# Kernel tuning notes

Hardware: AMD Instinct MI355X
Metric: run time of the kernel (lower is better)

The kernel has to match this reference:

```python
import jax, jax.numpy as jnp
import numpy as np

B, NW, WL, CH, D, H, L, FF = 8, 1024, 8, 4, 512, 8, 4, 2048
K = 512  # num_masked = int(0.5 * NW)
SCALE = (D // H) ** -0.5


def _ln(x, g, b):
    m = jnp.mean(x, -1, keepdims=True)
    v = jnp.var(x, -1, keepdims=True)
    return (x - m) * jax.lax.rsqrt(v + 1e-5) * g + b


def setup_inputs():
    key = jax.random.key(0)
    ks = jax.random.split(key, 16)
    n = lambda i, shape, s=0.02: jax.random.normal(ks[i], shape, jnp.float32) * s
    return {
        "seq": jax.random.normal(ks[0], (B, NW * WL, CH), jnp.float32),
        "mask_idx": jax.lax.top_k(jax.random.uniform(ks[1], (B, NW)), K)[1].astype(jnp.int32),
        "pos_embedding": n(2, (1, NW + 1, D)),
        "mask_token": jax.random.normal(ks[3], (D,), jnp.float32),
        "pln1_g": jnp.ones((WL * CH,)), "pln1_b": jnp.zeros((WL * CH,)),
        "W_emb": n(4, (WL * CH, D)), "b_emb": jnp.zeros((D,)),
        "pln2_g": jnp.ones((D,)), "pln2_b": jnp.zeros((D,)),
        "aln_g": jnp.ones((L, D)), "aln_b": jnp.zeros((L, D)),
        "Wqkv": n(5, (L, D, 3 * D)),
        "Wo": n(6, (L, D, D)),
        "fln_g": jnp.ones((L, D)), "fln_b": jnp.zeros((L, D)),
        "Wff1": n(7, (L, D, FF)), "bff1": jnp.zeros((L, FF)),
        "Wff2": n(8, (L, FF, D)), "bff2": jnp.zeros((L, D)),
        "oln_g": jnp.ones((D,)), "oln_b": jnp.zeros((D,)),
        "W_words": n(9, (D, WL * CH)), "b_words": jnp.zeros((WL * CH,)),
    }


def reference(seq, mask_idx, pos_embedding, mask_token, pln1_g, pln1_b, W_emb, b_emb,
              pln2_g, pln2_b, aln_g, aln_b, Wqkv, Wo, fln_g, fln_b, Wff1, bff1,
              Wff2, bff2, oln_g, oln_b, W_words, b_words):
    b = seq.shape[0]
    words = seq.reshape(b, NW, WL * CH)                       # to_patch: 'b (n w) c -> b n (w c)'
    pos = pos_embedding[:, 1:NW + 1]                          # [1, NW, D]
    tokens = _ln(_ln(words, pln1_g, pln1_b) @ W_emb + b_emb, pln2_g, pln2_b) + pos
    mask_tokens = mask_token + pos                            # [1, NW, D] broadcast over batch
    bool_mask = jnp.zeros((b, NW), bool).at[jnp.arange(b)[:, None], mask_idx].set(True)
    tokens = jnp.where(bool_mask[..., None], mask_tokens, tokens)

    def block(x, p):
        h = _ln(x, p["ag"], p["ab"])
        q, k, v = [t.reshape(b, NW, H, D // H) for t in jnp.split(h @ p["Wqkv"], 3, axis=-1)]
        attn = jax.nn.softmax(jnp.einsum("bihd,bjhd->bhij", q, k) * SCALE, axis=-1)
        o = jnp.einsum("bhij,bjhd->bihd", attn, v).reshape(b, NW, D)
        x = x + o @ p["Wo"]
        h = _ln(x, p["fg"], p["fb"])
        x = x + jax.nn.gelu(h @ p["W1"] + p["b1"]) @ p["W2"] + p["b2"]
        return x, None

    layer_params = {"ag": aln_g, "ab": aln_b, "Wqkv": Wqkv, "Wo": Wo,
                    "fg": fln_g, "fb": fln_b, "W1": Wff1, "b1": bff1,
                    "W2": Wff2, "b2": bff2}
    encoded, _ = jax.lax.scan(block, tokens, layer_params)
    encoded = _ln(encoded, oln_g, oln_b)

    idx = mask_idx[..., None]
    enc_m = jnp.take_along_axis(encoded, idx, axis=1)         # [b, K, D] gather of masked positions
    pred = jax.nn.softmax((enc_m @ W_words + b_words).reshape(b, K, WL, CH), axis=-1)
    labels = jnp.take_along_axis(words, idx, axis=1).reshape(b, K, WL, CH)
    return pred, labels
```

## Files before the change

### kernel.cpp

```cpp
#include <hip/hip_runtime.h>
#include <hip/hip_bf16.h>
#include <stdint.h>


#define NTOK 8192
#define DMODEL 512
#define NHEAD 8
#define DHEAD 64
#define NWIN 1024
#define NBATCH 8
#define KMASK 512
#define FFDIM 2048
#define NLAYER 4

typedef __bf16 bf16x8 __attribute__((ext_vector_type(8)));
typedef float f32x4 __attribute__((ext_vector_type(4)));

#define MFMA16(a, b, c) __builtin_amdgcn_mfma_f32_16x16x32_bf16(a, b, c, 0, 0, 0)

static __device__ __forceinline__ void gload_lds16(const void* g, void* l) {
    __builtin_amdgcn_global_load_lds(
        (const __attribute__((address_space(1))) uint32_t*)g,
        (__attribute__((address_space(3))) uint32_t*)l, 16, 0, 0);
}

static __device__ __forceinline__ float gelu_tanh(float v) {
    float x3 = v * v * v;
    return 0.5f * v * (1.f + tanhf(0.7978845608028654f * (v + 0.044715f * x3)));
}

__global__ void embed_kernel(const float* __restrict__ seq,
                             const float* __restrict__ pos_emb,
                             const float* __restrict__ pln1_g,
                             const float* __restrict__ pln1_b,
                             const float* __restrict__ W_emb,
                             const float* __restrict__ b_emb,
                             const float* __restrict__ pln2_g,
                             const float* __restrict__ pln2_b,
                             float* __restrict__ x) {
    int tok = blockIdx.x;
    int w = tok & (NWIN - 1);
    int t = threadIdx.x;

    __shared__ float wraw[32];
    __shared__ float ln1[32];
    __shared__ float red[256], red2[256];

    if (t < 32) wraw[t] = seq[(size_t)tok * 32 + t];
    __syncthreads();

    float m = 0.f;
    for (int j = 0; j < 32; j++) m += wraw[j];
    m *= (1.f / 32.f);
    float v = 0.f;
    for (int j = 0; j < 32; j++) { float d = wraw[j] - m; v += d * d; }
    v *= (1.f / 32.f);
    float rs = rsqrtf(v + 1e-5f);
    if (t < 32) ln1[t] = (wraw[t] - m) * rs * pln1_g[t] + pln1_b[t];
    __syncthreads();

    int c0 = t, c1 = t + 256;
    float e0 = b_emb[c0];
    float e1 = b_emb[c1];
    for (int j = 0; j < 32; j++) {
        float a = ln1[j];
        e0 += a * W_emb[j * DMODEL + c0];
        e1 += a * W_emb[j * DMODEL + c1];
    }

    red[t] = e0 + e1;
    red2[t] = e0 * e0 + e1 * e1;
    __syncthreads();
    for (int o = 128; o > 0; o >>= 1) {
        if (t < o) { red[t] += red[t + o]; red2[t] += red2[t + o]; }
        __syncthreads();
    }
    float mean = red[0] * (1.f / 512.f);
    float var = red2[0] * (1.f / 512.f) - mean * mean;
    float rs2 = rsqrtf(var + 1e-5f);

    const float* pr = pos_emb + (size_t)(1 + w) * DMODEL;
    x[(size_t)tok * DMODEL + c0] =
        (e0 - mean) * rs2 * pln2_g[c0] + pln2_b[c0] + pr[c0];
    x[(size_t)tok * DMODEL + c1] =
        (e1 - mean) * rs2 * pln2_g[c1] + pln2_b[c1] + pr[c1];
}

__global__ void mask_scatter_kernel(const int* __restrict__ mask_idx,
                                    const float* __restrict__ mask_token,
                                    const float* __restrict__ pos_emb,
                                    float* __restrict__ x) {
    int bk = blockIdx.x;
    int b = bk >> 9;
    int k = bk & 511;
    int idx = mask_idx[b * KMASK + k];
    int t = threadIdx.x;
    float* row = x + (size_t)(b * NWIN + idx) * DMODEL;
    const float* pr = pos_emb + (size_t)(1 + idx) * DMODEL;
    row[t]       = mask_token[t]       + pr[t];
    row[t + 256] = mask_token[t + 256] + pr[t + 256];
}

__global__ void ln_kernel(const float* __restrict__ in,
                          __hip_bfloat16* __restrict__ out,
                          const float* __restrict__ g,
                          const float* __restrict__ bb) {
    int row = blockIdx.x;
    int t = threadIdx.x;
    const float* r = in + (size_t)row * DMODEL;
    float v0 = r[t], v1 = r[t + 256];
    __shared__ float red[256], red2[256];
    red[t] = v0 + v1;
    red2[t] = v0 * v0 + v1 * v1;
    __syncthreads();
    for (int o = 128; o > 0; o >>= 1) {
        if (t < o) { red[t] += red[t + o]; red2[t] += red2[t + o]; }
        __syncthreads();
    }
    float mean = red[0] * (1.f / 512.f);
    float var = red2[0] * (1.f / 512.f) - mean * mean;
    float rs = rsqrtf(var + 1e-5f);
    out[(size_t)row * DMODEL + t] =
        __float2bfloat16((v0 - mean) * rs * g[t] + bb[t]);
    out[(size_t)row * DMODEL + t + 256] =
        __float2bfloat16((v1 - mean) * rs * g[t + 256] + bb[t + 256]);
}

__global__ void wconv_kernel(const float* __restrict__ src,
                             __hip_bfloat16* __restrict__ dst,
                             int K, int N) {
    int l = blockIdx.z;
    src += (size_t)l * K * N;
    dst += (size_t)l * K * N;
    __shared__ float t[32][33];
    int n0 = blockIdx.x * 32, k0 = blockIdx.y * 32;
    int tx = threadIdx.x & 31, ty = threadIdx.x >> 5;
    for (int p = 0; p < 4; p++) {
        int k = k0 + ty + p * 8;
        t[ty + p * 8][tx] = src[(size_t)k * N + n0 + tx];
    }
    __syncthreads();
    for (int p = 0; p < 4; p++) {
        int n = n0 + ty + p * 8;
        dst[(size_t)n * K + k0 + tx] = __float2bfloat16(t[tx][ty + p * 8]);
    }
}

static __device__ __forceinline__ void epi_store128(
        const float* Cs, int c, int m0, int n0, int N, int tid,
        const float* bias, const float* resid,
        float* Cf, __hip_bfloat16* Cb, int act) {
    int rl = tid >> 3;
    int cb = (tid & 7) * 16;
    int grow = m0 + c * 32 + rl;
    size_t base = (size_t)grow * N + n0 + cb;
    if (Cf) {
        for (int q = 0; q < 4; q++) {
            float4 v = *(const float4*)&Cs[rl * 132 + cb + q * 4];
            float vv[4] = {v.x, v.y, v.z, v.w};
            float4 ov;
            float* op = (float*)&ov;
            for (int e = 0; e < 4; e++) {
                float u = vv[e];
                if (bias) u += bias[n0 + cb + q * 4 + e];
                if (act == 1) u = gelu_tanh(u);
                if (resid) u += resid[base + q * 4 + e];
                op[e] = u;
            }
            *(float4*)&Cf[base + q * 4] = ov;
        }
    } else {
        for (int half = 0; half < 2; half++) {
            union { uint4 u; __hip_bfloat16 h[8]; } pk;
            for (int e = 0; e < 8; e++) {
                float u = Cs[rl * 132 + cb + half * 8 + e];
                if (bias) u += bias[n0 + cb + half * 8 + e];
                if (act == 1) u = gelu_tanh(u);
                pk.h[e] = __float2bfloat16(u);
            }
            *(uint4*)&Cb[base + half * 8] = pk.u;
        }
    }
}

static __device__ __forceinline__ void epi_store64(
        const float* Cs, int c, int m0, int n0, int N, int tid,
        const float* bias, const float* resid,
        float* Cf, __hip_bfloat16* Cb, int act) {
    int rl = tid >> 3;
    int cb = (tid & 7) * 8;
    int grow = m0 + c * 32 + rl;
    size_t base = (size_t)grow * N + n0 + cb;
    if (Cf) {
        for (int q = 0; q < 2; q++) {
            float4 v = *(const float4*)&Cs[rl * 68 + cb + q * 4];
            float vv[4] = {v.x, v.y, v.z, v.w};
            float4 ov;
            float* op = (float*)&ov;
            for (int e = 0; e < 4; e++) {
                float u = vv[e];
                if (bias) u += bias[n0 + cb + q * 4 + e];
                if (act == 1) u = gelu_tanh(u);
                if (resid) u += resid[base + q * 4 + e];
                op[e] = u;
            }
            *(float4*)&Cf[base + q * 4] = ov;
        }
    } else {
        union { uint4 u; __hip_bfloat16 h[8]; } pk;
        for (int e = 0; e < 8; e++) {
            float u = Cs[rl * 68 + cb + e];
            if (bias) u += bias[n0 + cb + e];
            if (act == 1) u = gelu_tanh(u);
            pk.h[e] = __float2bfloat16(u);
        }
        *(uint4*)&Cb[base] = pk.u;
    }
}

#define PUT128(ACC, II, JJ)                                             \
    do {                                                                \
        int rb_ = (II) * 16 + quad * 4;                                 \
        int cc_ = wc * 64 + (JJ) * 16 + l16;                            \
        Cs[(rb_ + 0) * 132 + cc_] = (ACC)[0];                           \
        Cs[(rb_ + 1) * 132 + cc_] = (ACC)[1];                           \
        Cs[(rb_ + 2) * 132 + cc_] = (ACC)[2];                           \
        Cs[(rb_ + 3) * 132 + cc_] = (ACC)[3];                           \
    } while (0)

#define CHUNK128(C, A00, A01, A02, A03, A10, A11, A12, A13)             \
    do {                                                                \
        __syncthreads();                                                \
        if (wr == ((C) >> 1)) {                                         \
            PUT128(A00, 0, 0); PUT128(A01, 0, 1);                       \
            PUT128(A02, 0, 2); PUT128(A03, 0, 3);                       \
            PUT128(A10, 1, 0); PUT128(A11, 1, 1);                       \
            PUT128(A12, 1, 2); PUT128(A13, 1, 3);                       \
        }                                                               \
        __syncthreads();                                                \
        epi_store128(Cs, (C), m0, n0, N, tid, bias, resid, Cf, Cb, act);\
    } while (0)

#define STAGE128(K0, BUF)                                               \
    do {                                                                \
        char* as_ = smem + (BUF) * 16384;                               \
        char* bs_ = as_ + 8192;                                         \
        _Pragma("unroll")                                               \
        for (int p_ = 0; p_ < 2; p_++) {                                \
            int row_ = wave * 32 + p_ * 16;                             \
            gload_lds16(Abase + (size_t)(p_ * 16) * (K * 2) + (K0) * 2, \
                        as_ + row_ * 64);                               \
            gload_lds16(Bbase + (size_t)(p_ * 16) * (K * 2) + (K0) * 2, \
                        bs_ + row_ * 64);                               \
        }                                                               \
    } while (0)

__global__ __launch_bounds__(256) void mfma_gemm_kernel(
        const __hip_bfloat16* __restrict__ A,
        const __hip_bfloat16* __restrict__ Bt,
        const float* __restrict__ bias,
        const float* __restrict__ resid,
        float* __restrict__ Cf,
        __hip_bfloat16* __restrict__ Cb,
        int N, int K, int act, int ntile) {
    __shared__ __align__(16) char smem[32768];
    float* Cs = (float*)smem;

    int tid = threadIdx.x;
    int wave = tid >> 6, lane = tid & 63;
    int quad = lane >> 4, l16 = lane & 15;
    int wr = wave >> 1, wc = wave & 1;

    int id = blockIdx.x;
    int slot = id >> 3;
    int mt = (id & 7) * 8 + slot / ntile;
    int nt = slot - (slot / ntile) * ntile;
    int m0 = mt * 128, n0 = nt * 128;

    f32x4 zero = {0.f, 0.f, 0.f, 0.f};
    f32x4 acc00 = zero, acc01 = zero, acc02 = zero, acc03 = zero;
    f32x4 acc10 = zero, acc11 = zero, acc12 = zero, acc13 = zero;
    f32x4 acc20 = zero, acc21 = zero, acc22 = zero, acc23 = zero;
    f32x4 acc30 = zero, acc31 = zero, acc32 = zero, acc33 = zero;

    int rsub = lane >> 2, csub = lane & 3;
    const char* Abase = (const char*)A +
        (size_t)(m0 + wave * 32 + rsub) * (K * 2) + csub * 16;
    const char* Bbase = (const char*)Bt +
        (size_t)(n0 + wave * 32 + rsub) * (K * 2) + csub * 16;

    int nit = K >> 5;
    STAGE128(0, 0);
    for (int it = 0; it < nit; it++) {
        __syncthreads();
        if (it + 1 < nit) STAGE128((it + 1) << 5, (it + 1) & 1);

        const __hip_bfloat16* as =
            (const __hip_bfloat16*)(smem + (it & 1) * 16384);
        const __hip_bfloat16* bs = as + 4096;

        bf16x8 a0 = *(const bf16x8*)&as[(wr * 64 +  0 + l16) * 32 + quad * 8];
        bf16x8 a1 = *(const bf16x8*)&as[(wr * 64 + 16 + l16) * 32 + quad * 8];
        bf16x8 a2 = *(const bf16x8*)&as[(wr * 64 + 32 + l16) * 32 + quad * 8];
        bf16x8 a3 = *(const bf16x8*)&as[(wr * 64 + 48 + l16) * 32 + quad * 8];
        bf16x8 b0 = *(const bf16x8*)&bs[(wc * 64 +  0 + l16) * 32 + quad * 8];
        bf16x8 b1 = *(const bf16x8*)&bs[(wc * 64 + 16 + l16) * 32 + quad * 8];
        bf16x8 b2 = *(const bf16x8*)&bs[(wc * 64 + 32 + l16) * 32 + quad * 8];
        bf16x8 b3 = *(const bf16x8*)&bs[(wc * 64 + 48 + l16) * 32 + quad * 8];

        acc00 = MFMA16(a0, b0, acc00); acc01 = MFMA16(a0, b1, acc01);
        acc02 = MFMA16(a0, b2, acc02); acc03 = MFMA16(a0, b3, acc03);
        acc10 = MFMA16(a1, b0, acc10); acc11 = MFMA16(a1, b1, acc11);
        acc12 = MFMA16(a1, b2, acc12); acc13 = MFMA16(a1, b3, acc13);
        acc20 = MFMA16(a2, b0, acc20); acc21 = MFMA16(a2, b1, acc21);
        acc22 = MFMA16(a2, b2, acc22); acc23 = MFMA16(a2, b3, acc23);
        acc30 = MFMA16(a3, b0, acc30); acc31 = MFMA16(a3, b1, acc31);
        acc32 = MFMA16(a3, b2, acc32); acc33 = MFMA16(a3, b3, acc33);
    }

    CHUNK128(0, acc00, acc01, acc02, acc03, acc10, acc11, acc12, acc13);
    CHUNK128(1, acc20, acc21, acc22, acc23, acc30, acc31, acc32, acc33);
    CHUNK128(2, acc00, acc01, acc02, acc03, acc10, acc11, acc12, acc13);
    CHUNK128(3, acc20, acc21, acc22, acc23, acc30, acc31, acc32, acc33);
}

#define PUT64(ACC, II, JJ)                                              \
    do {                                                                \
        int rb_ = (II) * 16 + quad * 4;                                 \
        int cc_ = (JJ) * 16 + l16;                                      \
        Cs[(rb_ + 0) * 68 + cc_] = (ACC)[0];                            \
        Cs[(rb_ + 1) * 68 + cc_] = (ACC)[1];                            \
        Cs[(rb_ + 2) * 68 + cc_] = (ACC)[2];                            \
        Cs[(rb_ + 3) * 68 + cc_] = (ACC)[3];                            \
    } while (0)

#define CHUNK64(C)                                                      \
    do {                                                                \
        __syncthreads();                                                \
        if (wave == (C)) {                                              \
            PUT64(acc00, 0, 0); PUT64(acc01, 0, 1);                     \
            PUT64(acc02, 0, 2); PUT64(acc03, 0, 3);                     \
            PUT64(acc10, 1, 0); PUT64(acc11, 1, 1);                     \
            PUT64(acc12, 1, 2); PUT64(acc13, 1, 3);                     \
        }                                                               \
        __syncthreads();                                                \
        epi_store64(Cs, (C), m0, n0, N, tid, bias, resid, Cf, Cb, act); \
    } while (0)

#define STAGE64(K0, BUF)                                                \
    do {                                                                \
        char* as_ = smem + (BUF) * 12288;                               \
        char* bs_ = as_ + 8192;                                         \
        _Pragma("unroll")                                               \
        for (int p_ = 0; p_ < 2; p_++) {                                \
            int row_ = wave * 32 + p_ * 16;                             \
            gload_lds16(Abase + (size_t)(p_ * 16) * (K * 2) + (K0) * 2, \
                        as_ + row_ * 64);                               \
        }                                                               \
        gload_lds16(Bbase + (K0) * 2, bs_ + (wave * 16) * 64);          \
    } while (0)

__global__ __launch_bounds__(256) void mfma_gemm_n64_kernel(
        const __hip_bfloat16* __restrict__ A,
        const __hip_bfloat16* __restrict__ Bt,
        const float* __restrict__ bias,
        const float* __restrict__ resid,
        float* __restrict__ Cf,
        __hip_bfloat16* __restrict__ Cb,
        int N, int K, int act, int ntile) {
    __shared__ __align__(16) char smem[24576];
    float* Cs = (float*)smem;

    int tid = threadIdx.x;
    int wave = tid >> 6, lane = tid & 63;
    int quad = lane >> 4, l16 = lane & 15;

    int id = blockIdx.x;
    int slot = id >> 3;
    int mt = (id & 7) * 8 + slot / ntile;
    int nt = slot - (slot / ntile) * ntile;
    int m0 = mt * 128, n0 = nt * 64;

    f32x4 zero = {0.f, 0.f, 0.f, 0.f};
    f32x4 acc00 = zero, acc01 = zero, acc02 = zero, acc03 = zero;
    f32x4 acc10 = zero, acc11 = zero, acc12 = zero, acc13 = zero;

    int rsub = lane >> 2, csub = lane & 3;
    const char* Abase = (const char*)A +
        (size_t)(m0 + wave * 32 + rsub) * (K * 2) + csub * 16;
    const char* Bbase = (const char*)Bt +
        (size_t)(n0 + wave * 16 + rsub) * (K * 2) + csub * 16;

    int nit = K >> 5;
    STAGE64(0, 0);
    for (int it = 0; it < nit; it++) {
        __syncthreads();
        if (it + 1 < nit) STAGE64((it + 1) << 5, (it + 1) & 1);

        const __hip_bfloat16* as =
            (const __hip_bfloat16*)(smem + (it & 1) * 12288);
        const __hip_bfloat16* bs = as + 4096;

        bf16x8 a0 = *(const bf16x8*)&as[(wave * 32 +  0 + l16) * 32 + quad * 8];
        bf16x8 a1 = *(const bf16x8*)&as[(wave * 32 + 16 + l16) * 32 + quad * 8];
        bf16x8 b0 = *(const bf16x8*)&bs[( 0 + l16) * 32 + quad * 8];
        bf16x8 b1 = *(const bf16x8*)&bs[(16 + l16) * 32 + quad * 8];
        bf16x8 b2 = *(const bf16x8*)&bs[(32 + l16) * 32 + quad * 8];
        bf16x8 b3 = *(const bf16x8*)&bs[(48 + l16) * 32 + quad * 8];

        acc00 = MFMA16(a0, b0, acc00); acc01 = MFMA16(a0, b1, acc01);
        acc02 = MFMA16(a0, b2, acc02); acc03 = MFMA16(a0, b3, acc03);
        acc10 = MFMA16(a1, b0, acc10); acc11 = MFMA16(a1, b1, acc11);
        acc12 = MFMA16(a1, b2, acc12); acc13 = MFMA16(a1, b3, acc13);
    }

    CHUNK64(0);
    CHUNK64(1);
    CHUNK64(2);
    CHUNK64(3);
}

#define KP 72
__global__ __launch_bounds__(256) void attn_mfma_kernel(
        const __hip_bfloat16* __restrict__ qkv,
        __hip_bfloat16* __restrict__ o) {
    int id = blockIdx.x;
    int slot = id >> 3;
    int bh = (id & 7) * 8 + (slot >> 3);
    int itile = slot & 7;
    int b = bh >> 3, hh = bh & 7;

    int tid = threadIdx.x;
    int wave = tid >> 6, lane = tid & 63;
    int quad = lane >> 4, l16 = lane & 15;
    int i0 = itile * 128;

    __shared__ __align__(16) __hip_bfloat16 Ks[64 * KP];
    __shared__ __align__(16) __hip_bfloat16 Vt[64 * KP];
    __shared__ __align__(16) __hip_bfloat16 Ps[4][16 * KP];

    bf16x8 aq[2][2];
#pragma unroll
    for (int g = 0; g < 2; g++) {
        const __hip_bfloat16* qrow =
            qkv + (size_t)(b * NWIN + i0 + g * 64 + wave * 16 + l16) * 1536 + hh * 64;
        aq[g][0] = *(const bf16x8*)(qrow + quad * 8);
        aq[g][1] = *(const bf16x8*)(qrow + 32 + quad * 8);
    }

    float lp[2][4];
    f32x4 acc[2][4];
    f32x4 zero = {0.f, 0.f, 0.f, 0.f};
#pragma unroll
    for (int g = 0; g < 2; g++)
#pragma unroll
        for (int n = 0; n < 4; n++) { acc[g][n] = zero; lp[g][n] = 0.f; }

    for (int kt = 0; kt < 16; kt++) {
        int k0 = kt * 64;
        __syncthreads();

#pragma unroll
        for (int p = 0; p < 2; p++) {
            int f = p * 256 + tid;
            int r = f >> 3;
            int j = f & 7;
            int c8 = j * 8;
            const __hip_bfloat16* kp =
                qkv + (size_t)(b * NWIN + k0 + r) * 1536 + 512 + hh * 64 + c8;
            *(uint4*)&Ks[r * KP + c8] = *(const uint4*)kp;
            union { uint4 u; __hip_bfloat16 h[8]; } vv;
            vv.u = *(const uint4*)(qkv + (size_t)(b * NWIN + k0 + r) * 1536 +
                                   1024 + hh * 64 + c8);
            int colb = (((r >> 3) ^ j) << 3) + (r & 7);
#pragma unroll
            for (int u = 0; u < 8; u++) Vt[(c8 + u) * KP + colb] = vv.h[u];
        }
        __syncthreads();

        bf16x8 bk[4][2], bv[4][2];
#pragma unroll
        for (int n = 0; n < 4; n++) {
            int key = n * 16 + l16;
            bk[n][0] = *(const bf16x8*)&Ks[key * KP + quad * 8];
            bk[n][1] = *(const bf16x8*)&Ks[key * KP + 32 + quad * 8];
            int d = n * 16 + l16;
            int sw = (d >> 3) & 7;
            bv[n][0] = *(const bf16x8*)&Vt[d * KP + ((quad ^ sw) << 3)];
            bv[n][1] = *(const bf16x8*)&Vt[d * KP + (((quad + 4) ^ sw) << 3)];
        }

#pragma unroll
        for (int g = 0; g < 2; g++) {
            f32x4 s[4];
#pragma unroll
            for (int n = 0; n < 4; n++) {
                f32x4 t = zero;
                t = MFMA16(aq[g][0], bk[n][0], t);
                t = MFMA16(aq[g][1], bk[n][1], t);
                s[n] = t;
            }
#pragma unroll
            for (int r = 0; r < 4; r++) {
                float ls = 0.f;
#pragma unroll
                for (int n = 0; n < 4; n++) {
                    float pv = __expf(s[n][r] * 0.125f);
                    Ps[wave][(quad * 4 + r) * KP + n * 16 + l16] =
                        __float2bfloat16(pv);
                    ls += pv;
                }
                lp[g][r] += ls;
            }
            bf16x8 ap0 = *(const bf16x8*)&Ps[wave][l16 * KP + quad * 8];
            bf16x8 ap1 = *(const bf16x8*)&Ps[wave][l16 * KP + 32 + quad * 8];
#pragma unroll
            for (int n = 0; n < 4; n++) {
                acc[g][n] = MFMA16(ap0, bv[n][0], acc[g][n]);
                acc[g][n] = MFMA16(ap1, bv[n][1], acc[g][n]);
            }
        }
    }

#pragma unroll
    for (int g = 0; g < 2; g++) {
#pragma unroll
        for (int r = 0; r < 4; r++) {
            float ls = lp[g][r];
            ls += __shfl_xor(ls, 1);
            ls += __shfl_xor(ls, 2);
            ls += __shfl_xor(ls, 4);
            ls += __shfl_xor(ls, 8);
            float invl = 1.f / ls;
            int row = i0 + g * 64 + wave * 16 + quad * 4 + r;
#pragma unroll
            for (int n = 0; n < 4; n++) {
                o[(size_t)(b * NWIN + row) * DMODEL + hh * 64 + n * 16 + l16] =
                    __float2bfloat16(acc[g][n][r] * invl);
            }
        }
    }
}

__global__ void out_kernel(const float* __restrict__ x,
                           const int* __restrict__ mask_idx,
                           const float* __restrict__ oln_g,
                           const float* __restrict__ oln_b,
                           const float* __restrict__ W_words,
                           const float* __restrict__ b_words,
                           const float* __restrict__ seq,
                           float* __restrict__ out) {
    int k = blockIdx.x, b = blockIdx.y;
    int idx = mask_idx[b * KMASK + k];
    int t = threadIdx.x;
    const float* row = x + (size_t)(b * NWIN + idx) * DMODEL;
    float v0 = row[t], v1 = row[t + 256];

    __shared__ float red[256], red2[256];
    __shared__ float sh[512];
    __shared__ float part[256];
    __shared__ float lg[32];

    red[t] = v0 + v1;
    red2[t] = v0 * v0 + v1 * v1;
    __syncthreads();
    for (int o = 128; o > 0; o >>= 1) {
        if (t < o) { red[t] += red[t + o]; red2[t] += red2[t + o]; }
        __syncthreads();
    }
    float mean = red[0] * (1.f / 512.f);
    float var = red2[0] * (1.f / 512.f) - mean * mean;
    float rs = rsqrtf(var + 1e-5f);
    sh[t]       = (v0 - mean) * rs * oln_g[t] + oln_b[t];
    sh[t + 256] = (v1 - mean) * rs * oln_g[t + 256] + oln_b[t + 256];
    __syncthreads();

    int c = t & 31, ch = t >> 5;
    float p = 0.f;
    for (int j = ch * 64; j < ch * 64 + 64; j++)
        p += sh[j] * W_words[j * 32 + c];
    part[t] = p;
    __syncthreads();
    if (t < 32) {
        float s = b_words[t];
        for (int u = 0; u < 8; u++) s += part[u * 32 + t];
        lg[t] = s;
    }
    __syncthreads();

    size_t obase = (size_t)(b * KMASK + k) * 32;
    if (t < 32) {
        int g0 = t & ~3;
        float mx = fmaxf(fmaxf(lg[g0], lg[g0 + 1]), fmaxf(lg[g0 + 2], lg[g0 + 3]));
        float s = expf(lg[g0] - mx) + expf(lg[g0 + 1] - mx) +
                  expf(lg[g0 + 2] - mx) + expf(lg[g0 + 3] - mx);
        out[obase + t] = expf(lg[t] - mx) / s;
        out[131072 + obase + t] = seq[(size_t)b * 32768 + (size_t)idx * 32 + t];
    }
}

extern "C" void kernel_launch(void* const* d_in, const int* in_sizes, int n_in,
                              void* d_out, int out_size, void* d_ws, size_t ws_size,
                              hipStream_t stream) {
    const float* seq      = (const float*)d_in[0];
    const int*   mask_idx = (const int*)d_in[1];
    const float* pos_emb  = (const float*)d_in[2];
    const float* mask_tok = (const float*)d_in[3];
    const float* pln1_g   = (const float*)d_in[4];
    const float* pln1_b   = (const float*)d_in[5];
    const float* W_emb    = (const float*)d_in[6];
    const float* b_emb    = (const float*)d_in[7];
    const float* pln2_g   = (const float*)d_in[8];
    const float* pln2_b   = (const float*)d_in[9];
    const float* aln_g    = (const float*)d_in[10];
    const float* aln_b    = (const float*)d_in[11];
    const float* Wqkv     = (const float*)d_in[12];
    const float* Wo       = (const float*)d_in[13];
    const float* fln_g    = (const float*)d_in[14];
    const float* fln_b    = (const float*)d_in[15];
    const float* Wff1     = (const float*)d_in[16];
    const float* bff1     = (const float*)d_in[17];
    const float* Wff2     = (const float*)d_in[18];
    const float* bff2     = (const float*)d_in[19];
    const float* oln_g    = (const float*)d_in[20];
    const float* oln_b    = (const float*)d_in[21];
    const float* W_words  = (const float*)d_in[22];
    const float* b_words  = (const float*)d_in[23];

    uint8_t* ws = (uint8_t*)d_ws;
    float* x = (float*)ws;
    __hip_bfloat16* qkv_bf = (__hip_bfloat16*)(ws + 16777216);
    __hip_bfloat16* ff_bf  = qkv_bf;
    __hip_bfloat16* h_bf   = (__hip_bfloat16*)(ws + 50331648);
    __hip_bfloat16* o_bf   = (__hip_bfloat16*)(ws + 58720256);
    __hip_bfloat16* wqkv_t = (__hip_bfloat16*)(ws + 67108864);
    __hip_bfloat16* wo_t   = wqkv_t + (size_t)NLAYER * DMODEL * 3 * DMODEL;
    __hip_bfloat16* wff1_t = wo_t   + (size_t)NLAYER * DMODEL * DMODEL;
    __hip_bfloat16* wff2_t = wff1_t + (size_t)NLAYER * DMODEL * FFDIM;

    wconv_kernel<<<dim3(48, 16, NLAYER), 256, 0, stream>>>(Wqkv, wqkv_t, DMODEL, 3 * DMODEL);
    wconv_kernel<<<dim3(16, 16, NLAYER), 256, 0, stream>>>(Wo,   wo_t,   DMODEL, DMODEL);
    wconv_kernel<<<dim3(64, 16, NLAYER), 256, 0, stream>>>(Wff1, wff1_t, DMODEL, FFDIM);
    wconv_kernel<<<dim3(16, 64, NLAYER), 256, 0, stream>>>(Wff2, wff2_t, FFDIM, DMODEL);

    embed_kernel<<<NTOK, 256, 0, stream>>>(seq, pos_emb, pln1_g, pln1_b,
                                           W_emb, b_emb, pln2_g, pln2_b, x);
    mask_scatter_kernel<<<NBATCH * KMASK, 256, 0, stream>>>(mask_idx, mask_tok, pos_emb, x);

    for (int l = 0; l < NLAYER; l++) {
        ln_kernel<<<NTOK, 256, 0, stream>>>(x, h_bf, aln_g + l * DMODEL, aln_b + l * DMODEL);
        mfma_gemm_kernel<<<64 * 12, 256, 0, stream>>>(
            h_bf, wqkv_t + (size_t)l * DMODEL * 3 * DMODEL,
            nullptr, nullptr, nullptr, qkv_bf, 3 * DMODEL, DMODEL, 0, 12);
        attn_mfma_kernel<<<512, 256, 0, stream>>>(qkv_bf, o_bf);
        mfma_gemm_n64_kernel<<<64 * 8, 256, 0, stream>>>(
            o_bf, wo_t + (size_t)l * DMODEL * DMODEL,
            nullptr, x, x, nullptr, DMODEL, DMODEL, 0, 8);
        ln_kernel<<<NTOK, 256, 0, stream>>>(x, h_bf, fln_g + l * DMODEL, fln_b + l * DMODEL);
        mfma_gemm_kernel<<<64 * 16, 256, 0, stream>>>(
            h_bf, wff1_t + (size_t)l * DMODEL * FFDIM,
            bff1 + (size_t)l * FFDIM, nullptr, nullptr, ff_bf, FFDIM, DMODEL, 1, 16);
        mfma_gemm_n64_kernel<<<64 * 8, 256, 0, stream>>>(
            ff_bf, wff2_t + (size_t)l * FFDIM * DMODEL,
            bff2 + (size_t)l * DMODEL, x, x, nullptr, DMODEL, FFDIM, 0, 8);
    }

    out_kernel<<<dim3(KMASK, NBATCH), 256, 0, stream>>>(
        x, mask_idx, oln_g, oln_b, W_words, b_words, seq, (float*)d_out);
}
```

Baseline: 897.9 us.

## Store GEMM tiles in MFMA fragment order, deepen n64 K-step, shuffle-reduce LayerNorm

The GEMM staging now writes each 16x32 sub-tile to LDS in the exact per-lane fragment order MFMA consumes, so each lane's LDS read is contiguous (lane*8) instead of row-strided. This is meant to remove LDS bank conflicts. The n64 GEMM kernel also processes 64 K per iteration with a doubled LDS buffer (48KB), which halves the number of barriers but may reduce occupancy. LayerNorm replaces its shared-memory tree reduction with wave shuffles and a single barrier.

```diff
diff --git a/kernel.cpp b/kernel.cpp
--- a/kernel.cpp
+++ b/kernel.cpp
@@ -109,16 +109,19 @@
     int t = threadIdx.x;
     const float* r = in + (size_t)row * DMODEL;
     float v0 = r[t], v1 = r[t + 256];
-    __shared__ float red[256], red2[256];
-    red[t] = v0 + v1;
-    red2[t] = v0 * v0 + v1 * v1;
-    __syncthreads();
-    for (int o = 128; o > 0; o >>= 1) {
-        if (t < o) { red[t] += red[t + o]; red2[t] += red2[t + o]; }
-        __syncthreads();
-    }
-    float mean = red[0] * (1.f / 512.f);
-    float var = red2[0] * (1.f / 512.f) - mean * mean;
+    float s = v0 + v1, s2 = v0 * v0 + v1 * v1;
+    for (int off = 1; off < 64; off <<= 1) {
+        s  += __shfl_xor(s, off);
+        s2 += __shfl_xor(s2, off);
+    }
+    __shared__ float ws[8];
+    int wave = t >> 6, lane = t & 63;
+    if (lane == 0) { ws[wave] = s; ws[4 + wave] = s2; }
+    __syncthreads();
+    float S  = ws[0] + ws[1] + ws[2] + ws[3];
+    float S2 = ws[4] + ws[5] + ws[6] + ws[7];
+    float mean = S * (1.f / 512.f);
+    float var = S2 * (1.f / 512.f) - mean * mean;
     float rs = rsqrtf(var + 1e-5f);
     out[(size_t)row * DMODEL + t] =
         __float2bfloat16((v0 - mean) * rs * g[t] + bb[t]);
@@ -247,11 +250,10 @@
         char* bs_ = as_ + 8192;                                         \
         _Pragma("unroll")                                               \
         for (int p_ = 0; p_ < 2; p_++) {                                \
-            int row_ = wave * 32 + p_ * 16;                             \
             gload_lds16(Abase + (size_t)(p_ * 16) * (K * 2) + (K0) * 2, \
-                        as_ + row_ * 64);                               \
+                        as_ + (wave * 2 + p_) * 1024);                  \
             gload_lds16(Bbase + (size_t)(p_ * 16) * (K * 2) + (K0) * 2, \
-                        bs_ + row_ * 64);                               \
+                        bs_ + (wave * 2 + p_) * 1024);                  \
         }                                                               \
     } while (0)
 
@@ -283,11 +285,10 @@
     f32x4 acc20 = zero, acc21 = zero, acc22 = zero, acc23 = zero;
     f32x4 acc30 = zero, acc31 = zero, acc32 = zero, acc33 = zero;
 
-    int rsub = lane >> 2, csub = lane & 3;
     const char* Abase = (const char*)A +
-        (size_t)(m0 + wave * 32 + rsub) * (K * 2) + csub * 16;
+        ((size_t)(m0 + wave * 32 + l16) * K + quad * 8) * 2;
     const char* Bbase = (const char*)Bt +
-        (size_t)(n0 + wave * 32 + rsub) * (K * 2) + csub * 16;
+        ((size_t)(n0 + wave * 32 + l16) * K + quad * 8) * 2;
 
     int nit = K >> 5;
     STAGE128(0, 0);
@@ -299,14 +300,14 @@
             (const __hip_bfloat16*)(smem + (it & 1) * 16384);
         const __hip_bfloat16* bs = as + 4096;
 
-        bf16x8 a0 = *(const bf16x8*)&as[(wr * 64 +  0 + l16) * 32 + quad * 8];
-        bf16x8 a1 = *(const bf16x8*)&as[(wr * 64 + 16 + l16) * 32 + quad * 8];
-        bf16x8 a2 = *(const bf16x8*)&as[(wr * 64 + 32 + l16) * 32 + quad * 8];
-        bf16x8 a3 = *(const bf16x8*)&as[(wr * 64 + 48 + l16) * 32 + quad * 8];
-        bf16x8 b0 = *(const bf16x8*)&bs[(wc * 64 +  0 + l16) * 32 + quad * 8];
-        bf16x8 b1 = *(const bf16x8*)&bs[(wc * 64 + 16 + l16) * 32 + quad * 8];
-        bf16x8 b2 = *(const bf16x8*)&bs[(wc * 64 + 32 + l16) * 32 + quad * 8];
-        bf16x8 b3 = *(const bf16x8*)&bs[(wc * 64 + 48 + l16) * 32 + quad * 8];
+        bf16x8 a0 = *(const bf16x8*)&as[(wr * 4 + 0) * 512 + lane * 8];
+        bf16x8 a1 = *(const bf16x8*)&as[(wr * 4 + 1) * 512 + lane * 8];
+        bf16x8 a2 = *(const bf16x8*)&as[(wr * 4 + 2) * 512 + lane * 8];
+        bf16x8 a3 = *(const bf16x8*)&as[(wr * 4 + 3) * 512 + lane * 8];
+        bf16x8 b0 = *(const bf16x8*)&bs[(wc * 4 + 0) * 512 + lane * 8];
+        bf16x8 b1 = *(const bf16x8*)&bs[(wc * 4 + 1) * 512 + lane * 8];
+        bf16x8 b2 = *(const bf16x8*)&bs[(wc * 4 + 2) * 512 + lane * 8];
+        bf16x8 b3 = *(const bf16x8*)&bs[(wc * 4 + 3) * 512 + lane * 8];
 
         acc00 = MFMA16(a0, b0, acc00); acc01 = MFMA16(a0, b1, acc01);
         acc02 = MFMA16(a0, b2, acc02); acc03 = MFMA16(a0, b3, acc03);
@@ -349,15 +350,22 @@
 
 #define STAGE64(K0, BUF)                                                \
     do {                                                                \
-        char* as_ = smem + (BUF) * 12288;                               \
-        char* bs_ = as_ + 8192;                                         \
+        char* as_ = smem + (BUF) * 24576;                               \
+        char* bs_ = as_ + 16384;                                        \
+        _Pragma("unroll")                                               \
+        for (int p_ = 0; p_ < 4; p_++) {                                \
+            int q_ = wave * 4 + p_;                                     \
+            gload_lds16(Abase + (size_t)((q_ & 7) * 16) * (K * 2)       \
+                              + ((K0) + (q_ >> 3) * 32) * 2,            \
+                        as_ + q_ * 1024);                               \
+        }                                                               \
         _Pragma("unroll")                                               \
         for (int p_ = 0; p_ < 2; p_++) {                                \
-            int row_ = wave * 32 + p_ * 16;                             \
-            gload_lds16(Abase + (size_t)(p_ * 16) * (K * 2) + (K0) * 2, \
-                        as_ + row_ * 64);                               \
+            int q_ = wave * 2 + p_;                                     \
+            gload_lds16(Bbase + (size_t)((q_ & 3) * 16) * (K * 2)       \
+                              + ((K0) + (q_ >> 2) * 32) * 2,            \
+                        bs_ + q_ * 1024);                               \
         }                                                               \
-        gload_lds16(Bbase + (K0) * 2, bs_ + (wave * 16) * 64);          \
     } while (0)
 
 __global__ __launch_bounds__(256) void mfma_gemm_n64_kernel(
@@ -368,7 +376,7 @@
         float* __restrict__ Cf,
         __hip_bfloat16* __restrict__ Cb,
         int N, int K, int act, int ntile) {
-    __shared__ __align__(16) char smem[24576];
+    __shared__ __align__(16) char smem[49152];
     float* Cs = (float*)smem;
 
     int tid = threadIdx.x;
@@ -385,33 +393,42 @@
     f32x4 acc00 = zero, acc01 = zero, acc02 = zero, acc03 = zero;
     f32x4 acc10 = zero, acc11 = zero, acc12 = zero, acc13 = zero;
 
-    int rsub = lane >> 2, csub = lane & 3;
     const char* Abase = (const char*)A +
-        (size_t)(m0 + wave * 32 + rsub) * (K * 2) + csub * 16;
+        ((size_t)(m0 + l16) * K + quad * 8) * 2;
     const char* Bbase = (const char*)Bt +
-        (size_t)(n0 + wave * 16 + rsub) * (K * 2) + csub * 16;
-
-    int nit = K >> 5;
+        ((size_t)(n0 + l16) * K + quad * 8) * 2;
+
+    int nit = K >> 6;
     STAGE64(0, 0);
     for (int it = 0; it < nit; it++) {
         __syncthreads();
-        if (it + 1 < nit) STAGE64((it + 1) << 5, (it + 1) & 1);
+        if (it + 1 < nit) STAGE64((it + 1) << 6, (it + 1) & 1);
 
         const __hip_bfloat16* as =
-            (const __hip_bfloat16*)(smem + (it & 1) * 12288);
-        const __hip_bfloat16* bs = as + 4096;
-
-        bf16x8 a0 = *(const bf16x8*)&as[(wave * 32 +  0 + l16) * 32 + quad * 8];
-        bf16x8 a1 = *(const bf16x8*)&as[(wave * 32 + 16 + l16) * 32 + quad * 8];
-        bf16x8 b0 = *(const bf16x8*)&bs[( 0 + l16) * 32 + quad * 8];
-        bf16x8 b1 = *(const bf16x8*)&bs[(16 + l16) * 32 + quad * 8];
-        bf16x8 b2 = *(const bf16x8*)&bs[(32 + l16) * 32 + quad * 8];
-        bf16x8 b3 = *(const bf16x8*)&bs[(48 + l16) * 32 + quad * 8];
-
-        acc00 = MFMA16(a0, b0, acc00); acc01 = MFMA16(a0, b1, acc01);
-        acc02 = MFMA16(a0, b2, acc02); acc03 = MFMA16(a0, b3, acc03);
-        acc10 = MFMA16(a1, b0, acc10); acc11 = MFMA16(a1, b1, acc11);
-        acc12 = MFMA16(a1, b2, acc12); acc13 = MFMA16(a1, b3, acc13);
+            (const __hip_bfloat16*)(smem + (it & 1) * 24576);
+        const __hip_bfloat16* bs = as + 8192;
+
+        bf16x8 a0h0 = *(const bf16x8*)&as[(0 * 8 + wave * 2 + 0) * 512 + lane * 8];
+        bf16x8 a1h0 = *(const bf16x8*)&as[(0 * 8 + wave * 2 + 1) * 512 + lane * 8];
+        bf16x8 a0h1 = *(const bf16x8*)&as[(1 * 8 + wave * 2 + 0) * 512 + lane * 8];
+        bf16x8 a1h1 = *(const bf16x8*)&as[(1 * 8 + wave * 2 + 1) * 512 + lane * 8];
+        bf16x8 b0h0 = *(const bf16x8*)&bs[(0 * 4 + 0) * 512 + lane * 8];
+        bf16x8 b1h0 = *(const bf16x8*)&bs[(0 * 4 + 1) * 512 + lane * 8];
+        bf16x8 b2h0 = *(const bf16x8*)&bs[(0 * 4 + 2) * 512 + lane * 8];
+        bf16x8 b3h0 = *(const bf16x8*)&bs[(0 * 4 + 3) * 512 + lane * 8];
+        bf16x8 b0h1 = *(const bf16x8*)&bs[(1 * 4 + 0) * 512 + lane * 8];
+        bf16x8 b1h1 = *(const bf16x8*)&bs[(1 * 4 + 1) * 512 + lane * 8];
+        bf16x8 b2h1 = *(const bf16x8*)&bs[(1 * 4 + 2) * 512 + lane * 8];
+        bf16x8 b3h1 = *(const bf16x8*)&bs[(1 * 4 + 3) * 512 + lane * 8];
+
+        acc00 = MFMA16(a0h0, b0h0, acc00); acc01 = MFMA16(a0h0, b1h0, acc01);
+        acc02 = MFMA16(a0h0, b2h0, acc02); acc03 = MFMA16(a0h0, b3h0, acc03);
+        acc10 = MFMA16(a1h0, b0h0, acc10); acc11 = MFMA16(a1h0, b1h0, acc11);
+        acc12 = MFMA16(a1h0, b2h0, acc12); acc13 = MFMA16(a1h0, b3h0, acc13);
+        acc00 = MFMA16(a0h1, b0h1, acc00); acc01 = MFMA16(a0h1, b1h1, acc01);
+        acc02 = MFMA16(a0h1, b2h1, acc02); acc03 = MFMA16(a0h1, b3h1, acc03);
+        acc10 = MFMA16(a1h1, b0h1, acc10); acc11 = MFMA16(a1h1, b1h1, acc11);
+        acc12 = MFMA16(a1h1, b2h1, acc12); acc13 = MFMA16(a1h1, b3h1, acc13);
     }
 
     CHUNK64(0);
```

Result: slower. 1.070 ms (+19.1%).
